# Kernel tuning notes

Hardware: AMD Instinct MI355X
Metric: run time of the kernel (lower is better)

## Reference

```python
import jax, jax.numpy as jnp
import numpy as np

K = 16  # neighbors (module's self.k)


def _gather(points, idx):
    # points (B,C,N), idx (B,M[,k]) -> (B,C,M[,k])
    return jax.vmap(lambda p, i: p[:, i])(points, idx)


def _fps(xyz, nsample):
    # furthest point sampling on xyz (B,3,N) -> idx (B,nsample) int32
    B, _, N = xyz.shape

    def body(carry, _):
        dists, last = carry
        lp = jnp.take_along_axis(xyz, last[:, None, None], axis=2)  # (B,3,1)
        d = jnp.sum((xyz - lp) ** 2, axis=1)  # (B,N)
        dists = jnp.minimum(dists, d)
        nxt = jnp.argmax(dists, axis=1).astype(jnp.int32)
        return (dists, nxt), nxt

    init_idx = jnp.zeros((B,), dtype=jnp.int32)
    init_d = jnp.full((B, N), jnp.finfo(xyz.dtype).max, xyz.dtype)
    _, rest = jax.lax.scan(body, (init_d, init_idx), None, length=nsample - 1)
    return jnp.concatenate([init_idx[None], rest], axis=0).T  # (B,nsample)


def _knn(query, points, k):
    # query (B,C,M), points (B,C,N): k nearest in feature space
    d = (jnp.sum(query ** 2, axis=1)[:, :, None]
         + jnp.sum(points ** 2, axis=1)[:, None, :]
         - 2.0 * jnp.einsum('bcm,bcn->bmn', query, points))  # (B,M,N)
    _, idx = jax.lax.top_k(-d, k)  # (B,M,k)
    return _gather(points, idx), idx  # (B,C,M,k), (B,M,k)


def _conv1x1(W, b, y):
    # y (B,Cin,M,k), W (Cout,Cin) -> (B,Cout,M,k)
    return jnp.einsum('oi,bimk->bomk', W, y) + b[None, :, None, None]


def setup_inputs() -> dict:
    key = jax.random.key(0)
    ks = jax.random.split(key, 8)
    B, C, N = 4, 64, 8192
    g = 64
    return {
        'x': jax.random.normal(ks[0], (B, C, N), jnp.float32),
        'xyz': jax.random.normal(ks[1], (B, 3, N), jnp.float32),
        'W0': jax.random.normal(ks[2], (g, 2 * C), jnp.float32) * 0.05,
        'b0': jax.random.normal(ks[3], (g,), jnp.float32) * 0.05,
        'W1': jax.random.normal(ks[4], (g, C + g), jnp.float32) * 0.05,
        'b1': jax.random.normal(ks[5], (g,), jnp.float32) * 0.05,
        'W2': jax.random.normal(ks[6], (g, C + 2 * g), jnp.float32) * 0.05,
        'b2': jax.random.normal(ks[7], (g,), jnp.float32) * 0.05,
        'nsample': 2048,
    }


def reference(x, xyz, W0, b0, W1, b1, W2, b2, nsample):
    # furthest point sample on coordinates, gather sampled features
    sampled_idx = _fps(xyz, nsample)              # (B,M)
    sampled_xyz = _gather(xyz, sampled_idx)       # (B,3,M)
    sampled_x = _gather(x, sampled_idx)           # (B,C,M)
    # local graph: k+1 NN in feature space, drop self
    knn_pt, _ = _knn(sampled_x, x, K + 1)
    knn_pt = knn_pt[..., 1:]                      # (B,C,M,K)
    center = sampled_x[..., None]                 # (B,C,M,1)
    center_k = jnp.broadcast_to(center, knn_pt.shape)
    edge = jnp.concatenate([center_k, knn_pt - center_k], axis=1)  # (B,2C,M,K)
    # dense edge conv cascade
    y = jnp.concatenate([jax.nn.relu(_conv1x1(W0, b0, edge)), center_k], axis=1)
    y = jnp.concatenate([jax.nn.relu(_conv1x1(W1, b1, y)), y], axis=1)
    y = jnp.concatenate([_conv1x1(W2, b2, y), y], axis=1)
    y = jnp.max(y, axis=-1)                       # (B, C+3*g, M)
    return (y, sampled_xyz, sampled_idx)
```

## Files before the change

kernel.cpp:

```cpp
#include <hip/hip_runtime.h>
#include <hip/hip_bf16.h>
#include <stdint.h>

typedef unsigned long long u64;
typedef unsigned int u32;
typedef unsigned short u16;

#define B_   4
#define C_   64
#define N_   8192
#define M_   2048
#define KNB  16
#define FLT_MAX_ 3.402823466e+38f
#define SMEM_SZ 87296

__device__ __forceinline__ int clampN(int v) {
    return v < 0 ? 0 : (v > N_ - 1 ? N_ - 1 : v);
}


__device__ __forceinline__ void pin4(float4& v) {
    asm volatile("" : "+v"(v.x), "+v"(v.y), "+v"(v.z), "+v"(v.w));
}

__device__ __forceinline__ float wave_fmax_dpp(float v) {
    float t;
    t = __int_as_float(__builtin_amdgcn_update_dpp(0, __float_as_int(v), 0x111, 0xf, 0xf, true)); v = fmaxf(v, t);
    t = __int_as_float(__builtin_amdgcn_update_dpp(0, __float_as_int(v), 0x112, 0xf, 0xf, true)); v = fmaxf(v, t);
    t = __int_as_float(__builtin_amdgcn_update_dpp(0, __float_as_int(v), 0x114, 0xf, 0xf, true)); v = fmaxf(v, t);
    t = __int_as_float(__builtin_amdgcn_update_dpp(0, __float_as_int(v), 0x118, 0xf, 0xf, true)); v = fmaxf(v, t);
    t = __int_as_float(__builtin_amdgcn_update_dpp(0, __float_as_int(v), 0x142, 0xa, 0xf, true)); v = fmaxf(v, t);
    t = __int_as_float(__builtin_amdgcn_update_dpp(0, __float_as_int(v), 0x143, 0xc, 0xf, true)); v = fmaxf(v, t);
    return __int_as_float(__builtin_amdgcn_readlane(__float_as_int(v), 63));
}

#define FPS_STEP(PX, PY, PZ, DD, J)                                          \
    {                                                                        \
        float dx = __fsub_rn((PX), lx);                                      \
        float dy = __fsub_rn((PY), ly);                                      \
        float dz = __fsub_rn((PZ), lz);                                      \
        float d = __fadd_rn(__fadd_rn(__fmul_rn(dx, dx), __fmul_rn(dy, dy)), \
                            __fmul_rn(dz, dz));                              \
        float nd = fminf((DD), d);                                           \
        (DD) = nd;                                                           \
        bool gt = nd > fm;                                                   \
        fm = gt ? nd : fm;                                                   \
        fj = gt ? (J) : fj;                                                  \
        fx = gt ? (PX) : fx;                                                 \
        fy = gt ? (PY) : fy;                                                 \
        fz = gt ? (PZ) : fz;                                                 \
    }

__global__ void init_kernel(u32* __restrict__ flags) {
    if (threadIdx.x < 16) flags[threadIdx.x] = 0;
}

__global__ __launch_bounds__(512, 2) void mega_kernel(
    const float* __restrict__ xyz, const float* __restrict__ x,
    const float* __restrict__ W0, const float* __restrict__ W1,
    const float* __restrict__ W2, u16* __restrict__ idx_ws,
    float* __restrict__ pnorm_ws, float* __restrict__ wt,
    float* __restrict__ out1, float* __restrict__ out2,
    u16* __restrict__ nbr_ws, u32* __restrict__ flags) {
    const int bid = blockIdx.x;
    const int tid = threadIdx.x;
    __shared__ __align__(16) char SM[SMEM_SZ];

    if (bid < 4) {
        const int b = bid;
        const int lane = tid & 63;
        const int w = tid >> 6;
        const float* xb = xyz + b * 3 * N_;
        const int n0 = tid * 16;

        float4* red4 = (float4*)SM;
        int*    redi = (int*)(SM + 256);
        u16*    hist = (u16*)(SM + 320);

        float4 px[4], py[4], pz[4], dd[4];
#pragma unroll
        for (int j4 = 0; j4 < 4; ++j4) {
            px[j4] = *(const float4*)(xb + n0 + j4 * 4);
            py[j4] = *(const float4*)(xb + N_ + n0 + j4 * 4);
            pz[j4] = *(const float4*)(xb + 2 * N_ + n0 + j4 * 4);
            pin4(px[j4]); pin4(py[j4]); pin4(pz[j4]);
            dd[j4] = make_float4(FLT_MAX_, FLT_MAX_, FLT_MAX_, FLT_MAX_);
        }

        int cur = 0;
        float lx = xb[0], ly = xb[N_], lz = xb[2 * N_];
        if (tid == 0) { idx_ws[b * M_ + 0] = 0; hist[0] = 0; }

        for (int s = 1; s < M_; ++s) {
            float fm = -1.0f, fx = 0.f, fy = 0.f, fz = 0.f;
            int fj = 0;
#pragma unroll
            for (int j4 = 0; j4 < 4; ++j4) {
                FPS_STEP(px[j4].x, py[j4].x, pz[j4].x, dd[j4].x, j4 * 4 + 0);
                FPS_STEP(px[j4].y, py[j4].y, pz[j4].y, dd[j4].y, j4 * 4 + 1);
                FPS_STEP(px[j4].z, py[j4].z, pz[j4].z, dd[j4].z, j4 * 4 + 2);
                FPS_STEP(px[j4].w, py[j4].w, pz[j4].w, dd[j4].w, j4 * 4 + 3);
            }
            float wm = wave_fmax_dpp(fm);
            u64 bal = __ballot(fm == wm);
            int winlane = (int)__ffsll(bal) - 1;
            const int par = s & 1;
            if (lane == winlane) {
                red4[(par << 3) + w] = make_float4(wm, fx, fy, fz);
                redi[(par << 3) + w] = n0 + fj;
            }
            __syncthreads();
            float4 p0 = red4[par << 3];
            float g = p0.x; float nlx = p0.y, nly = p0.z, nlz = p0.w;
            int ncur = redi[par << 3];
#pragma unroll
            for (int ww = 1; ww < 8; ++ww) {
                float4 p = red4[(par << 3) + ww];
                int id = redi[(par << 3) + ww];
                bool gt = p.x > g;
                g = gt ? p.x : g;
                nlx = gt ? p.y : nlx; nly = gt ? p.z : nly; nlz = gt ? p.w : nlz;
                ncur = gt ? id : ncur;
            }
            lx = nlx; ly = nly; lz = nlz; cur = ncur;
            if (tid == 0) {
                idx_ws[b * M_ + s] = (u16)cur; hist[s] = (u16)cur;
                if ((s & 63) == 63)
                    __hip_atomic_store(&flags[b], (u32)s, __ATOMIC_RELEASE,
                                       __HIP_MEMORY_SCOPE_AGENT);
            }
        }

        __syncthreads();
        for (int m = tid; m < M_; m += 512) {
            int idx = (int)hist[m];
            out2[b * M_ + m] = (float)idx;
            out1[(b * 3 + 0) * M_ + m] = xb[idx];
            out1[(b * 3 + 1) * M_ + m] = xb[N_ + idx];
            out1[(b * 3 + 2) * M_ + m] = xb[2 * N_ + idx];
        }
        return;
    }

    if (bid < 68) {
        int gid = (bid - 4) * 512 + tid;
        int bb = gid >> 13, n = gid & 8191;
        const float* xb = x + bb * C_ * N_ + n;
        float acc = 0.f;
#pragma unroll 16
        for (int c = 0; c < C_; ++c) { float v = xb[c * N_]; acc = fmaf(v, v, acc); }
        pnorm_ws[gid] = acc;
        __syncthreads();
        if (tid == 0)
            __hip_atomic_fetch_add(&flags[4], 1u, __ATOMIC_RELEASE,
                                   __HIP_MEMORY_SCOPE_AGENT);
        return;
    }

    if (bid < 124) {
        int e = (bid - 68) * 512 + tid;
        if (e < 8192) {
            int i = e >> 6, o = e & 63;
            wt[e] = W0[o * 128 + i];
        } else if (e < 16384) {
            int e2 = e - 8192; int i = e2 >> 6, o = e2 & 63;
            wt[8192 + e2] = W1[o * 128 + i];
        } else {
            int e2 = e - 16384; int i = e2 >> 6, o = e2 & 63;
            wt[16384 + e2] = W2[o * 192 + i];
        }
        return;
    }

    {
        const int kid = bid - 124;
        const int b = kid >> 6;
        const int m0 = (kid & 63) * 32;

        float* pt    = (float*)SM;
        float* spn   = (float*)(SM + 17408);
        u64*   lists = (u64*)(SM + 17664);

        if (tid == 0) {
            while (__hip_atomic_load(&flags[4], __ATOMIC_ACQUIRE,
                                     __HIP_MEMORY_SCOPE_AGENT) < 64u)
                __builtin_amdgcn_s_sleep(2);
            const u32 need = (u32)(m0 + 31);
            while (__hip_atomic_load(&flags[b], __ATOMIC_ACQUIRE,
                                     __HIP_MEMORY_SCOPE_AGENT) < need)
                __builtin_amdgcn_s_sleep(2);
        }
        __syncthreads();

        const int q = tid & 31, sub = tid >> 5;
        const int m = m0 + q;
        const float* xb = x + b * C_ * N_;
        const int self = clampN((int)idx_ws[b * M_ + m]);

        float4 qv[16];
#pragma unroll
        for (int c4 = 0; c4 < 16; ++c4) {
            qv[c4].x = xb[(c4 * 4 + 0) * N_ + self];
            qv[c4].y = xb[(c4 * 4 + 1) * N_ + self];
            qv[c4].z = xb[(c4 * 4 + 2) * N_ + self];
            qv[c4].w = xb[(c4 * 4 + 3) * N_ + self];
        }
        const float qn = pnorm_ws[b * N_ + self];

        u64* L = lists + tid * 17;
#pragma unroll
        for (int j = 0; j < 17; ++j) L[j] = ~0ULL;
        u64 worst = ~0ULL;

        for (int t = 0; t < N_ / 64; ++t) {
            const int nb0 = t * 64;
            __syncthreads();
#pragma unroll
            for (int r = 0; r < 2; ++r) {
                int e = tid + r * 512;
                int c = e >> 4, nq = e & 15;
                float4 v = *(const float4*)(xb + c * N_ + nb0 + nq * 4);
                const int cs = c ^ (nq << 2);
                pt[(nq * 4 + 0) * 68 + cs] = v.x;
                pt[(nq * 4 + 1) * 68 + cs] = v.y;
                pt[(nq * 4 + 2) * 68 + cs] = v.z;
                pt[(nq * 4 + 3) * 68 + cs] = v.w;
            }
            if (tid < 64) spn[tid] = pnorm_ws[b * N_ + nb0 + tid];
            __syncthreads();
#pragma unroll
            for (int pp = 0; pp < 4; ++pp) {
                int nl = sub * 4 + pp;
                const float* pvbase = pt + nl * 68;
                const int rsw = (nl >> 2) << 2;
                float a0 = 0.f, a1 = 0.f, a2 = 0.f, a3 = 0.f;
#pragma unroll
                for (int c4 = 0; c4 < 16; ++c4) {
                    float4 p = *(const float4*)(pvbase + (((c4 << 2) ^ rsw)));
                    a0 = fmaf(qv[c4].x, p.x, a0);
                    a1 = fmaf(qv[c4].y, p.y, a1);
                    a2 = fmaf(qv[c4].z, p.z, a2);
                    a3 = fmaf(qv[c4].w, p.w, a3);
                }
                float dot = (a0 + a1) + (a2 + a3);
                float d = qn + spn[nl] - 2.0f * dot;
                u32 db = __float_as_uint(d);
                db = (db & 0x80000000u) ? ~db : (db | 0x80000000u);
                u64 key = ((u64)db << 32) | (u32)(nb0 + nl);
                if (key < worst) {
                    int j = 16;
                    while (j > 0 && L[j - 1] > key) { L[j] = L[j - 1]; --j; }
                    L[j] = key;
                    worst = L[16];
                }
            }
        }
        __syncthreads();
        if (tid < 32) {
            int pos[16];
#pragma unroll
            for (int s2 = 0; s2 < 16; ++s2) pos[s2] = 0;
            u16* outp = nbr_ws + (b * M_ + m0 + tid) * KNB;
            for (int r = 0; r < 17; ++r) {
                u64 best = ~0ULL; int bs = 0;
#pragma unroll
                for (int s2 = 0; s2 < 16; ++s2) {
                    u64 k2 = (pos[s2] < 17) ? lists[(tid + 32 * s2) * 17 + pos[s2]] : ~0ULL;
                    if (k2 < best) { best = k2; bs = s2; }
                }
#pragma unroll
                for (int s2 = 0; s2 < 16; ++s2) pos[s2] += (s2 == bs) ? 1 : 0;
                if (r > 0) outp[r - 1] = (u16)clampN((int)(best & 0xFFFFFFFFu));
            }
        }
    }
}

__device__ __forceinline__ void mm_tile(float a[4][4], const float* __restrict__ w,
                                        const float* __restrict__ s, int ni) {
#pragma unroll 8
    for (int i = 0; i < ni; ++i) {
        const float4 w4 = *(const float4*)(w + i * 64);
        const float4 e4 = *(const float4*)(s + i * 64);
        a[0][0] = fmaf(w4.x, e4.x, a[0][0]);
        a[0][1] = fmaf(w4.x, e4.y, a[0][1]);
        a[0][2] = fmaf(w4.x, e4.z, a[0][2]);
        a[0][3] = fmaf(w4.x, e4.w, a[0][3]);
        a[1][0] = fmaf(w4.y, e4.x, a[1][0]);
        a[1][1] = fmaf(w4.y, e4.y, a[1][1]);
        a[1][2] = fmaf(w4.y, e4.z, a[1][2]);
        a[1][3] = fmaf(w4.y, e4.w, a[1][3]);
        a[2][0] = fmaf(w4.z, e4.x, a[2][0]);
        a[2][1] = fmaf(w4.z, e4.y, a[2][1]);
        a[2][2] = fmaf(w4.z, e4.z, a[2][2]);
        a[2][3] = fmaf(w4.z, e4.w, a[2][3]);
        a[3][0] = fmaf(w4.w, e4.x, a[3][0]);
        a[3][1] = fmaf(w4.w, e4.y, a[3][1]);
        a[3][2] = fmaf(w4.w, e4.z, a[3][2]);
        a[3][3] = fmaf(w4.w, e4.w, a[3][3]);
    }
}

__global__ __launch_bounds__(256) void conv_kernel(const float* __restrict__ x,
                                                   const u16* __restrict__ idx_ws,
                                                   const u16* __restrict__ nbr_ws,
                                                   const float* __restrict__ wt,
                                                   const float* __restrict__ bias0,
                                                   const float* __restrict__ bias1,
                                                   const float* __restrict__ bias2,
                                                   float* __restrict__ out0) {
    __shared__ float E[128 * 64];
    __shared__ float H0[64 * 64];

    const int tid = threadIdx.x;
    const int b = blockIdx.x >> 9;
    const int m0 = (blockIdx.x & 511) * 4;
    const float* xb = x + b * C_ * N_;

    {
        const int col = tid & 63;
        const int half = tid >> 6;
        const int m = m0 + (col >> 4);
        const int k = col & 15;
        const int selfm = clampN((int)idx_ws[b * M_ + m]);
        const int nbr = clampN((int)nbr_ws[(b * M_ + m) * KNB + k]);
#pragma unroll
        for (int c2 = 0; c2 < 16; ++c2) {
            int c = half * 16 + c2;
            float ctr = xb[c * N_ + selfm];
            float nb = xb[c * N_ + nbr];
            E[c * 64 + col] = ctr;
            E[(64 + c) * 64 + col] = __fsub_rn(nb, ctr);
        }
    }
    __syncthreads();

    const int o0 = (tid >> 4) * 4;
    const int c0 = (tid & 15) * 4;
    float a[4][4];

    {
        float4 bb = *(const float4*)(bias0 + o0);
        a[0][0] = a[0][1] = a[0][2] = a[0][3] = bb.x;
        a[1][0] = a[1][1] = a[1][2] = a[1][3] = bb.y;
        a[2][0] = a[2][1] = a[2][2] = a[2][3] = bb.z;
        a[3][0] = a[3][1] = a[3][2] = a[3][3] = bb.w;
        mm_tile(a, wt + o0, E + c0, 128);
#pragma unroll
        for (int oo = 0; oo < 4; ++oo) {
            float4 v = make_float4(fmaxf(a[oo][0], 0.f), fmaxf(a[oo][1], 0.f),
                                   fmaxf(a[oo][2], 0.f), fmaxf(a[oo][3], 0.f));
            *(float4*)(H0 + (o0 + oo) * 64 + c0) = v;
        }
    }
    __syncthreads();

    {
        float4 bb = *(const float4*)(bias1 + o0);
        a[0][0] = a[0][1] = a[0][2] = a[0][3] = bb.x;
        a[1][0] = a[1][1] = a[1][2] = a[1][3] = bb.y;
        a[2][0] = a[2][1] = a[2][2] = a[2][3] = bb.z;
        a[3][0] = a[3][1] = a[3][2] = a[3][3] = bb.w;
        mm_tile(a, wt + 8192 + o0, H0 + c0, 64);
        mm_tile(a, wt + 8192 + 64 * 64 + o0, E + c0, 64);
#pragma unroll
        for (int oo = 0; oo < 4; ++oo) {
            float4 v = make_float4(fmaxf(a[oo][0], 0.f), fmaxf(a[oo][1], 0.f),
                                   fmaxf(a[oo][2], 0.f), fmaxf(a[oo][3], 0.f));
            *(float4*)(E + (64 + o0 + oo) * 64 + c0) = v;
        }
    }
    __syncthreads();

    {
        float4 bb = *(const float4*)(bias2 + o0);
        a[0][0] = a[0][1] = a[0][2] = a[0][3] = bb.x;
        a[1][0] = a[1][1] = a[1][2] = a[1][3] = bb.y;
        a[2][0] = a[2][1] = a[2][2] = a[2][3] = bb.z;
        a[3][0] = a[3][1] = a[3][2] = a[3][3] = bb.w;
        mm_tile(a, wt + 16384 + o0, E + 64 * 64 + c0, 64);
        mm_tile(a, wt + 16384 + 64 * 64 + o0, H0 + c0, 64);
        mm_tile(a, wt + 16384 + 128 * 64 + o0, E + c0, 64);
    }

#pragma unroll
    for (int r = 1; r < 4; ++r) {
        int e = tid + r * 256;
        int ch = e >> 2, mloc = e & 3;
        int colb = mloc * 16;
        float v;
        if (ch < 128) {
            const float* row = E + (64 + (ch - 64)) * 64 + colb;
            v = row[0];
#pragma unroll
            for (int k = 1; k < 16; ++k) v = fmaxf(v, row[k]);
        } else if (ch < 192) {
            const float* row = H0 + (ch - 128) * 64 + colb;
            v = row[0];
#pragma unroll
            for (int k = 1; k < 16; ++k) v = fmaxf(v, row[k]);
        } else {
            v = E[(ch - 192) * 64 + colb];
        }
        out0[((b * 256 + ch) << 11) + m0 + mloc] = v;
    }
    __syncthreads();

    {
#pragma unroll
        for (int oo = 0; oo < 4; ++oo) {
            float4 v = make_float4(a[oo][0], a[oo][1], a[oo][2], a[oo][3]);
            *(float4*)(E + (64 + o0 + oo) * 64 + c0) = v;
        }
    }
    __syncthreads();

    {
        int ch = tid >> 2, mloc = tid & 3;
        int colb = mloc * 16;
        const float* row = E + (64 + ch) * 64 + colb;
        float v = row[0];
#pragma unroll
        for (int k = 1; k < 16; ++k) v = fmaxf(v, row[k]);
        out0[((b * 256 + ch) << 11) + m0 + mloc] = v;
    }
}

extern "C" void kernel_launch(void* const* d_in, const int* in_sizes, int n_in,
                              void* d_out, int out_size, void* d_ws, size_t ws_size,
                              hipStream_t stream) {
    const float* x   = (const float*)d_in[0];
    const float* xyz = (const float*)d_in[1];
    const float* W0  = (const float*)d_in[2];
    const float* b0  = (const float*)d_in[3];
    const float* W1  = (const float*)d_in[4];
    const float* b1  = (const float*)d_in[5];
    const float* W2  = (const float*)d_in[6];
    const float* b2  = (const float*)d_in[7];

    float* out  = (float*)d_out;
    float* out0 = out;
    float* out1 = out + 4 * 256 * 2048;
    float* out2 = out1 + 4 * 3 * 2048;
    u32*   flags = (u32*)out0;

    char* ws = (char*)d_ws;
    u16*   idx_ws   = (u16*)ws;
    u16*   nbr_ws   = (u16*)(ws + 16384);
    float* pnorm_ws = (float*)(ws + 278528);
    float* wt_ws    = (float*)(ws + 409600);

    init_kernel<<<1, 64, 0, stream>>>(flags);
    mega_kernel<<<380, 512, 0, stream>>>(xyz, x, W0, W1, W2,
                                         idx_ws, pnorm_ws, wt_ws,
                                         out1, out2, nbr_ws, flags);
    conv_kernel<<<2048, 256, 0, stream>>>(x, idx_ws, nbr_ws, wt_ws,
                                          b0, b1, b2, out0);
}
```

Measured before the change: 2.854 ms.

## Split KNN search over point range into four partial blocks with merge kernel

Result: faster. 2.439 ms (-14.5%).

```diff
diff --git a/kernel.cpp b/kernel.cpp
--- a/kernel.cpp
+++ b/kernel.cpp
@@ -13,6 +13,7 @@
 #define KNB  16
 #define FLT_MAX_ 3.402823466e+38f
 #define SMEM_SZ 87296
+#define NSPLIT 4
 
 __device__ __forceinline__ int clampN(int v) {
     return v < 0 ? 0 : (v > N_ - 1 ? N_ - 1 : v);
@@ -61,7 +62,7 @@
     const float* __restrict__ W2, u16* __restrict__ idx_ws,
     float* __restrict__ pnorm_ws, float* __restrict__ wt,
     float* __restrict__ out1, float* __restrict__ out2,
-    u16* __restrict__ nbr_ws, u32* __restrict__ flags) {
+    u64* __restrict__ part, u32* __restrict__ flags) {
     const int bid = blockIdx.x;
     const int tid = threadIdx.x;
     __shared__ __align__(16) char SM[SMEM_SZ];
@@ -174,8 +175,10 @@
 
     {
         const int kid = bid - 124;
-        const int b = kid >> 6;
-        const int m0 = (kid & 63) * 32;
+        const int grp = kid >> 4;
+        const int b   = (kid >> 2) & 3;
+        const int sp  = kid & 3;
+        const int m0  = grp * 32;
 
         float* pt    = (float*)SM;
         float* spn   = (float*)(SM + 17408);
@@ -212,7 +215,7 @@
         for (int j = 0; j < 17; ++j) L[j] = ~0ULL;
         u64 worst = ~0ULL;
 
-        for (int t = 0; t < N_ / 64; ++t) {
+        for (int t = sp * 32; t < sp * 32 + 32; ++t) {
             const int nb0 = t * 64;
             __syncthreads();
 #pragma unroll
@@ -260,7 +263,7 @@
             int pos[16];
 #pragma unroll
             for (int s2 = 0; s2 < 16; ++s2) pos[s2] = 0;
-            u16* outp = nbr_ws + (b * M_ + m0 + tid) * KNB;
+            u64* outp = part + (((u64)(b * M_ + m0 + tid)) * NSPLIT + sp) * 17;
             for (int r = 0; r < 17; ++r) {
                 u64 best = ~0ULL; int bs = 0;
 #pragma unroll
@@ -270,9 +273,31 @@
                 }
 #pragma unroll
                 for (int s2 = 0; s2 < 16; ++s2) pos[s2] += (s2 == bs) ? 1 : 0;
-                if (r > 0) outp[r - 1] = (u16)clampN((int)(best & 0xFFFFFFFFu));
-            }
-        }
+                outp[r] = best;
+            }
+        }
+    }
+}
+
+__global__ __launch_bounds__(512) void knn_merge_kernel(const u64* __restrict__ part,
+                                                        u16* __restrict__ nbr_ws) {
+    int gid = blockIdx.x * 512 + threadIdx.x;
+    const u64* p0 = part + ((u64)gid * NSPLIT + 0) * 17;
+    const u64* p1 = p0 + 17;
+    const u64* p2 = p1 + 17;
+    const u64* p3 = p2 + 17;
+    int i0 = 0, i1 = 0, i2 = 0, i3 = 0;
+    u16* outp = nbr_ws + gid * KNB;
+    for (int r = 0; r < 17; ++r) {
+        u64 k0 = p0[i0], k1 = p1[i1], k2 = p2[i2], k3 = p3[i3];
+        u64 ka = k0 < k1 ? k0 : k1;
+        u64 kb = k2 < k3 ? k2 : k3;
+        u64 best = ka < kb ? ka : kb;
+        i0 += (best == k0) ? 1 : 0;
+        i1 += (best == k1 && best != k0) ? 1 : 0;
+        i2 += (best == k2 && best != k0 && best != k1) ? 1 : 0;
+        i3 += (best == k3 && best != k0 && best != k1 && best != k2) ? 1 : 0;
+        if (r > 0) outp[r - 1] = (u16)clampN((int)(best & 0xFFFFFFFFu));
     }
 }
 
@@ -443,6 +468,7 @@
     float* out1 = out + 4 * 256 * 2048;
     float* out2 = out1 + 4 * 3 * 2048;
     u32*   flags = (u32*)out0;
+    u64*   part  = (u64*)(out0 + 262144);
 
     char* ws = (char*)d_ws;
     u16*   idx_ws   = (u16*)ws;
@@ -451,9 +477,10 @@
     float* wt_ws    = (float*)(ws + 409600);
 
     init_kernel<<<1, 64, 0, stream>>>(flags);
-    mega_kernel<<<380, 512, 0, stream>>>(xyz, x, W0, W1, W2,
-                                         idx_ws, pnorm_ws, wt_ws,
-                                         out1, out2, nbr_ws, flags);
+    mega_kernel<<<1148, 512, 0, stream>>>(xyz, x, W0, W1, W2,
+                                          idx_ws, pnorm_ws, wt_ws,
+                                          out1, out2, part, flags);
+    knn_merge_kernel<<<16, 512, 0, stream>>>(part, nbr_ws);
     conv_kernel<<<2048, 256, 0, stream>>>(x, idx_ws, nbr_ws, wt_ws,
                                           b0, b1, b2, out0);
 }
```

## Split KNN scan over N into eight partial blocks and merge separately

Applied to the files above, without the earlier changes.

Result: faster. 2.444 ms (-14.4%).

```diff
diff --git a/kernel.cpp b/kernel.cpp
--- a/kernel.cpp
+++ b/kernel.cpp
@@ -13,6 +13,7 @@
 #define KNB  16
 #define FLT_MAX_ 3.402823466e+38f
 #define SMEM_SZ 87296
+#define NSPLIT 8
 
 __device__ __forceinline__ int clampN(int v) {
     return v < 0 ? 0 : (v > N_ - 1 ? N_ - 1 : v);
@@ -61,7 +62,8 @@
     const float* __restrict__ W2, u16* __restrict__ idx_ws,
     float* __restrict__ pnorm_ws, float* __restrict__ wt,
     float* __restrict__ out1, float* __restrict__ out2,
-    u16* __restrict__ nbr_ws, u32* __restrict__ flags) {
+    u32* __restrict__ part_hi, u16* __restrict__ part_lo,
+    u32* __restrict__ flags) {
     const int bid = blockIdx.x;
     const int tid = threadIdx.x;
     __shared__ __align__(16) char SM[SMEM_SZ];
@@ -174,8 +176,10 @@
 
     {
         const int kid = bid - 124;
-        const int b = kid >> 6;
-        const int m0 = (kid & 63) * 32;
+        const int grp = kid >> 5;
+        const int b   = (kid >> 3) & 3;
+        const int sp  = kid & 7;
+        const int m0  = grp * 32;
 
         float* pt    = (float*)SM;
         float* spn   = (float*)(SM + 17408);
@@ -212,22 +216,37 @@
         for (int j = 0; j < 17; ++j) L[j] = ~0ULL;
         u64 worst = ~0ULL;
 
-        for (int t = 0; t < N_ / 64; ++t) {
+        const int tF = sp * 16, tL = tF + 16;
+        const int cA = tid >> 4, nqA = tid & 15, csA = cA ^ (nqA << 2);
+        const int eB = tid + 512;
+        const int cB = eB >> 4, nqB = eB & 15, csB = cB ^ (nqB << 2);
+        const float* pA = xb + cA * N_ + nqA * 4;
+        const float* pB = xb + cB * N_ + nqB * 4;
+
+        float4 s0 = *(const float4*)(pA + tF * 64);
+        float4 s1 = *(const float4*)(pB + tF * 64);
+        float sv = (tid < 64) ? pnorm_ws[b * N_ + tF * 64 + tid] : 0.f;
+
+        for (int t = tF; t < tL; ++t) {
+            __syncthreads();
+            pt[(nqA * 4 + 0) * 68 + csA] = s0.x;
+            pt[(nqA * 4 + 1) * 68 + csA] = s0.y;
+            pt[(nqA * 4 + 2) * 68 + csA] = s0.z;
+            pt[(nqA * 4 + 3) * 68 + csA] = s0.w;
+            pt[(nqB * 4 + 0) * 68 + csB] = s1.x;
+            pt[(nqB * 4 + 1) * 68 + csB] = s1.y;
+            pt[(nqB * 4 + 2) * 68 + csB] = s1.z;
+            pt[(nqB * 4 + 3) * 68 + csB] = s1.w;
+            if (tid < 64) spn[tid] = sv;
+            float4 n0 = make_float4(0.f, 0.f, 0.f, 0.f), n1 = n0;
+            float nv = 0.f;
+            if (t + 1 < tL) {
+                n0 = *(const float4*)(pA + (t + 1) * 64);
+                n1 = *(const float4*)(pB + (t + 1) * 64);
+                if (tid < 64) nv = pnorm_ws[b * N_ + (t + 1) * 64 + tid];
+            }
+            __syncthreads();
             const int nb0 = t * 64;
-            __syncthreads();
-#pragma unroll
-            for (int r = 0; r < 2; ++r) {
-                int e = tid + r * 512;
-                int c = e >> 4, nq = e & 15;
-                float4 v = *(const float4*)(xb + c * N_ + nb0 + nq * 4);
-                const int cs = c ^ (nq << 2);
-                pt[(nq * 4 + 0) * 68 + cs] = v.x;
-                pt[(nq * 4 + 1) * 68 + cs] = v.y;
-                pt[(nq * 4 + 2) * 68 + cs] = v.z;
-                pt[(nq * 4 + 3) * 68 + cs] = v.w;
-            }
-            if (tid < 64) spn[tid] = pnorm_ws[b * N_ + nb0 + tid];
-            __syncthreads();
 #pragma unroll
             for (int pp = 0; pp < 4; ++pp) {
                 int nl = sub * 4 + pp;
@@ -254,13 +273,14 @@
                     worst = L[16];
                 }
             }
+            s0 = n0; s1 = n1; sv = nv;
         }
         __syncthreads();
         if (tid < 32) {
             int pos[16];
 #pragma unroll
             for (int s2 = 0; s2 < 16; ++s2) pos[s2] = 0;
-            u16* outp = nbr_ws + (b * M_ + m0 + tid) * KNB;
+            const u32 base = (u32)(((b * M_ + m0 + tid) * NSPLIT + sp) * 17);
             for (int r = 0; r < 17; ++r) {
                 u64 best = ~0ULL; int bs = 0;
 #pragma unroll
@@ -270,9 +290,35 @@
                 }
 #pragma unroll
                 for (int s2 = 0; s2 < 16; ++s2) pos[s2] += (s2 == bs) ? 1 : 0;
-                if (r > 0) outp[r - 1] = (u16)clampN((int)(best & 0xFFFFFFFFu));
-            }
-        }
+                part_hi[base + r] = (u32)(best >> 32);
+                part_lo[base + r] = (u16)(best & 0xFFFFu);
+            }
+        }
+    }
+}
+
+__global__ __launch_bounds__(512) void knn_merge_kernel(const u32* __restrict__ part_hi,
+                                                        const u16* __restrict__ part_lo,
+                                                        u16* __restrict__ nbr_ws) {
+    int gid = blockIdx.x * 512 + threadIdx.x;
+    const u32* ph = part_hi + (u64)gid * NSPLIT * 17;
+    const u16* pl = part_lo + (u64)gid * NSPLIT * 17;
+    int pos[NSPLIT];
+#pragma unroll
+    for (int s = 0; s < NSPLIT; ++s) pos[s] = 0;
+    u16* outp = nbr_ws + gid * KNB;
+    for (int r = 0; r < 17; ++r) {
+        u64 best = ~0ULL; int bs = 0;
+#pragma unroll
+        for (int s = 0; s < NSPLIT; ++s) {
+            int p = pos[s];
+            u64 k = (p < 17) ? ((((u64)ph[s * 17 + p]) << 32) | (u64)pl[s * 17 + p])
+                             : ~0ULL;
+            if (k < best) { best = k; bs = s; }
+        }
+#pragma unroll
+        for (int s = 0; s < NSPLIT; ++s) pos[s] += (s == bs) ? 1 : 0;
+        if (r > 0) outp[r - 1] = (u16)clampN((int)(best & 0xFFFFu));
     }
 }
 
@@ -442,7 +488,9 @@
     float* out0 = out;
     float* out1 = out + 4 * 256 * 2048;
     float* out2 = out1 + 4 * 3 * 2048;
-    u32*   flags = (u32*)out0;
+    u32*   flags   = (u32*)out0;
+    u32*   part_hi = (u32*)(out0 + 16);
+    u16*   part_lo = (u16*)(part_hi + 8192 * NSPLIT * 17);
 
     char* ws = (char*)d_ws;
     u16*   idx_ws   = (u16*)ws;
@@ -451,9 +499,10 @@
     float* wt_ws    = (float*)(ws + 409600);
 
     init_kernel<<<1, 64, 0, stream>>>(flags);
-    mega_kernel<<<380, 512, 0, stream>>>(xyz, x, W0, W1, W2,
-                                         idx_ws, pnorm_ws, wt_ws,
-                                         out1, out2, nbr_ws, flags);
+    mega_kernel<<<2172, 512, 0, stream>>>(xyz, x, W0, W1, W2,
+                                          idx_ws, pnorm_ws, wt_ws,
+                                          out1, out2, part_hi, part_lo, flags);
+    knn_merge_kernel<<<16, 512, 0, stream>>>(part_hi, part_lo, nbr_ws);
     conv_kernel<<<2048, 256, 0, stream>>>(x, idx_ws, nbr_ws, wt_ws,
                                           b0, b1, b2, out0);
 }
```
